# Optimization experiments

Hardware: AMD Instinct MI355X
Metric: run time of the kernel (lower is better)

Reference implementation:

```python
import jax, jax.numpy as jnp
import numpy as np

HEAD_DIM = 64
EMB_DIM = 1024
BATCH = 4
SEQ = 4096


def setup_inputs() -> dict:
    key = jax.random.key(0)
    kx, kq, kk, kv = jax.random.split(key, 4)
    scale = 1.0 / np.sqrt(EMB_DIM)
    x = jax.random.normal(kx, (BATCH, SEQ, EMB_DIM), dtype=jnp.float32)
    # nn.Linear(emb_dim, head_dim, bias=False): weight [head_dim, emb_dim]; store transposed [emb_dim, head_dim]
    Wq = jax.random.normal(kq, (EMB_DIM, HEAD_DIM), dtype=jnp.float32) * scale
    Wk = jax.random.normal(kk, (EMB_DIM, HEAD_DIM), dtype=jnp.float32) * scale
    Wv = jax.random.normal(kv, (EMB_DIM, HEAD_DIM), dtype=jnp.float32) * scale
    return {"x": x, "Wq": Wq, "Wk": Wk, "Wv": Wv}


def reference(x, Wq, Wk, Wv):
    # x: [b, s, e] -> q,k,v: [b, s, d]
    q = jnp.einsum("bse,ed->bsd", x, Wq)
    k = jnp.einsum("bse,ed->bsd", x, Wk)
    v = jnp.einsum("bse,ed->bsd", x, Wv)
    d = q.shape[-1]
    # scores: [b, s, s], scaled by 1/sqrt(head_dim)
    scores = jnp.einsum("bqd,bkd->bqk", q, k) / jnp.sqrt(jnp.asarray(d, q.dtype))
    s = x.shape[1]
    causal = jnp.tril(jnp.ones((s, s), dtype=bool))
    scores = jnp.where(causal, scores, jnp.asarray(-jnp.inf, scores.dtype))
    attn = jax.nn.softmax(scores, axis=-1)
    return jnp.einsum("bqk,bkd->bqd", attn, v)
```

## Files before the change

kernel.cpp:

```cpp
#include <hip/hip_runtime.h>
#include <hip/hip_bf16.h>
#include <math.h>

#define BATCH 4
#define SEQ   4096
#define EMB   1024
#define HD    64

#define QBLK  64
#define KBLK  64
#define CHUNK 512
#define BM    16

#define NSPB  288
#define NSLOT (BATCH * NSPB)

#define SCL   0.1803368801111204f

typedef _Float16 half8 __attribute__((ext_vector_type(8)));
typedef _Float16 half4 __attribute__((ext_vector_type(4)));
typedef float    f32x4 __attribute__((ext_vector_type(4)));

#define GLOAD_LDS16(g, l) __builtin_amdgcn_global_load_lds(                 \
    (const __attribute__((address_space(1))) void*)(g),                     \
    (__attribute__((address_space(3))) void*)(l), 16, 0, 0)

#define DPPF(v, ctrl) __int_as_float(__builtin_amdgcn_update_dpp(           \
    0, __float_as_int(v), ctrl, 0xF, 0xF, true))

static __device__ __forceinline__ float bf2f(unsigned int u16) {
    union { unsigned int i; float f; } v;
    v.i = u16 << 16;
    return v.f;
}

__global__ void detect_dtype(const unsigned short* __restrict__ x,
                             int* __restrict__ flag)
{
    const int tid = threadIdx.x;
    int big = 0;
    for (int i = tid; i < 2048; i += 64) {
        const int e = (x[i] >> 7) & 0xff;
        if (e > 146) big++;
    }
    #pragma unroll
    for (int off = 32; off; off >>= 1) big += __shfl_xor(big, off);
    if (tid == 0) *flag = (big > 200) ? 0 : 1;
}

__global__ __launch_bounds__(256) void w_to_fp16t(
    const void* __restrict__ Wqp, const void* __restrict__ Wkp,
    const void* __restrict__ Wvp, const int* __restrict__ flagp,
    _Float16* __restrict__ Wt)
{
    const int gid = blockIdx.x * 256 + threadIdx.x;
    const int n   = gid >> 7;
    const int kc  = (gid & 127) << 3;
    const int mat = n >> 6, d = n & 63;
    const void* Wp = (mat == 0) ? Wqp : (mat == 1 ? Wkp : Wvp);

    half8 o;
    if (*flagp) {
        const unsigned short* W = (const unsigned short*)Wp;
        #pragma unroll
        for (int j = 0; j < 8; ++j) o[j] = (_Float16)bf2f(W[(kc + j) * HD + d]);
    } else {
        const float* W = (const float*)Wp;
        #pragma unroll
        for (int j = 0; j < 8; ++j) o[j] = (_Float16)W[(kc + j) * HD + d];
    }
    const int tk = kc >> 5;
    *(half8*)&Wt[((tk * 192) + n) * 32 + (kc & 31)] = o;
}

__global__ __launch_bounds__(256) void qkv_gemm(
    const void* __restrict__ xp, const _Float16* __restrict__ Wt,
    const int* __restrict__ flagp,
    _Float16* __restrict__ Qh, _Float16* __restrict__ Kh,
    _Float16* __restrict__ Vth)
{
    __shared__ _Float16 Xs[2][BM * 64];

    const int tid  = threadIdx.x;
    const int w    = tid >> 6;
    const int lane = tid & 63;
    const int c15  = lane & 15;
    const int kg   = lane >> 4;
    const size_t row0 = (size_t)blockIdx.x * BM;
    const int isbf = *flagp;

    const bool st = tid < 128;
    const int sr = (tid >> 3) & 15, ss = tid & 7;
    const size_t gbase = (row0 + sr) * EMB + ss * 8;
    const int lidx = sr * 64 + ((ss ^ (sr & 7)) << 3);

    const int wtbase = (w * 48 + c15) * 32 + kg * 8;

    float4 f0[2], f1[2];
    uint4  u0,    u1;

    auto ldc = [&](int t, float4* f, uint4* u) {
        if (!st) return;
        if (isbf) *u = *(const uint4*)((const unsigned short*)xp + gbase + t * 64);
        else {
            f[0] = *(const float4*)((const float*)xp + gbase + t * 64);
            f[1] = *(const float4*)((const float*)xp + gbase + t * 64 + 4);
        }
    };
    auto wrc = [&](int buf, const float4* f, const uint4* u) {
        if (!st) return;
        half8 h;
        if (isbf) {
            const unsigned int uu[4] = {u->x, u->y, u->z, u->w};
            #pragma unroll
            for (int q = 0; q < 4; ++q) {
                h[2 * q]     = (_Float16)bf2f(uu[q] & 0xffffu);
                h[2 * q + 1] = (_Float16)bf2f(uu[q] >> 16);
            }
        } else {
            const float ff[8] = {f[0].x, f[0].y, f[0].z, f[0].w,
                                 f[1].x, f[1].y, f[1].z, f[1].w};
            #pragma unroll
            for (int q = 0; q < 8; ++q) h[q] = (_Float16)ff[q];
        }
        *(half8*)&Xs[buf][lidx] = h;
    };

    half8 bf0[6], bf1[6];
    auto ldb = [&](int t, half8* bf) {
        #pragma unroll
        for (int kk = 0; kk < 2; ++kk)
            #pragma unroll
            for (int nf = 0; nf < 3; ++nf)
                bf[kk * 3 + nf] = *(const half8*)&Wt[
                    (t * 2 + kk) * 192 * 32 + nf * 16 * 32 + wtbase];
    };

    f32x4 acc[3];
    #pragma unroll
    for (int nf = 0; nf < 3; ++nf) acc[nf] = (f32x4){0.f, 0.f, 0.f, 0.f};

    auto compute = [&](int buf, const half8* bf) {
        #pragma unroll
        for (int kk = 0; kk < 2; ++kk) {
            const half8 a = *(const half8*)&Xs[buf][c15 * 64 +
                            (((kk * 4 + kg) ^ (c15 & 7)) << 3)];
            #pragma unroll
            for (int nf = 0; nf < 3; ++nf)
                acc[nf] = __builtin_amdgcn_mfma_f32_16x16x32_f16(
                    a, bf[kk * 3 + nf], acc[nf], 0, 0, 0);
        }
    };

    ldc(0, f0, &u0);
    ldb(0, bf0);
    wrc(0, f0, &u0);
    ldc(1, f1, &u1);

    for (int tt = 0; tt < 16; tt += 2) {
        __syncthreads();
        if (tt + 2 < 16) ldc(tt + 2, f0, &u0);
        ldb(tt + 1, bf1);
        compute(0, bf0);
        wrc(1, f1, &u1);
        __syncthreads();
        if (tt + 3 < 16) ldc(tt + 3, f1, &u1);
        if (tt + 2 < 16) ldb(tt + 2, bf0);
        compute(1, bf1);
        if (tt + 2 < 16) wrc(0, f0, &u0);
    }

    #pragma unroll
    for (int nf = 0; nf < 3; ++nf) {
        const int nc  = w * 48 + nf * 16;
        const int mat = nc >> 6;
        const int d   = (nc & 63) + c15;
        if (mat < 2) {
            _Float16* Out = mat ? Kh : Qh;
            const float qs = mat ? 1.f : SCL;
            #pragma unroll
            for (int r = 0; r < 4; ++r)
                Out[(row0 + kg * 4 + r) * HD + d] = (_Float16)(acc[nf][r] * qs);
        } else {
            const int bb = (int)(row0 >> 12);
            const int s0 = (int)(row0 & 4095);
            half4 hv;
            #pragma unroll
            for (int r = 0; r < 4; ++r) hv[r] = (_Float16)acc[nf][r];
            *(half4*)&Vth[((size_t)bb * HD + d) * SEQ + s0 + kg * 4] = hv;
        }
    }
}

__global__ __launch_bounds__(256) void attn_split(
    const _Float16* __restrict__ Qh, const _Float16* __restrict__ Kh,
    const _Float16* __restrict__ Vth,
    _Float16* __restrict__ PoG, float* __restrict__ PmG,
    float* __restrict__ PlG)
{
    __shared__ _Float16 Kt[2][KBLK * HD];
    __shared__ _Float16 Vt[2][HD * KBLK];
    __shared__ _Float16 Ps[4][16 * KBLK];

    const int b = blockIdx.y;
    const int f = blockIdx.x;
    int c = 0, off = 0, cnt = 64;
    while (f >= off + cnt) { off += cnt; ++c; cnt -= 8; }
    const int qb = 8 * c + (f - off);
    const int q0 = qb * QBLK;
    const int kstart = c * CHUNK;
    const int kend   = min(kstart + CHUNK, q0 + QBLK);
    const int nt     = (kend - kstart) / KBLK;

    const int tid  = threadIdx.x;
    const int w    = tid >> 6;
    const int lane = tid & 63;
    const int col  = lane & 15;
    const int kg   = lane >> 4;

    const size_t bo = (size_t)b * SEQ;
    const _Float16* Kb = Kh + bo * HD;
    const _Float16* Vb = Vth + (size_t)b * HD * SEQ;

    const _Float16* Qp = Qh + (bo + q0 + w * 16 + col) * HD;
    const half8 aq0 = *(const half8*)(Qp + kg * 8);
    const half8 aq1 = *(const half8*)(Qp + 32 + kg * 8);

    half8 vone;
    #pragma unroll
    for (int j = 0; j < 8; ++j) vone[j] = (_Float16)1.0f;

    f32x4 O[4];
    f32x4 Ls = (f32x4){0.f, 0.f, 0.f, 0.f};
    float mreg[4];
    #pragma unroll
    for (int cq = 0; cq < 4; ++cq) O[cq] = (f32x4){0.f, 0.f, 0.f, 0.f};
    #pragma unroll
    for (int r = 0; r < 4; ++r) mreg[r] = -INFINITY;

    const int wh = w & 1;
    auto stage = [&](int t, int buf) {
        const int k0 = kstart + t * KBLK;
        if (w < 2) {
            const _Float16* g = Kb + (size_t)k0 * HD;
            #pragma unroll
            for (int i = 0; i < 4; ++i) {
                const int c2 = (wh * 4 + i) * 64 + lane;
                const int key = c2 >> 3, slot = c2 & 7;
                GLOAD_LDS16(g + key * HD + ((slot ^ (key & 7)) << 3),
                            &Kt[buf][(wh * 4 + i) * 512]);
            }
        } else {
            const _Float16* g = Vb + k0;
            #pragma unroll
            for (int i = 0; i < 4; ++i) {
                const int c2 = (wh * 4 + i) * 64 + lane;
                const int dim = c2 >> 3, slot = c2 & 7;
                GLOAD_LDS16(g + (size_t)dim * SEQ + ((slot ^ (dim & 7)) << 3),
                            &Vt[buf][(wh * 4 + i) * 512]);
            }
        }
    };

    stage(0, 0);
    int cur = 0;

    for (int t = 0; t < nt; ++t) {
        __syncthreads();
        if (t + 1 < nt) stage(t + 1, cur ^ 1);

        const int k0 = kstart + t * KBLK;

        f32x4 S[4];
        __builtin_amdgcn_s_setprio(1);
        #pragma unroll
        for (int cq = 0; cq < 4; ++cq) {
            const int key = cq * 16 + col;
            const int sw  = key & 7;
            const half8 bk0 = *(const half8*)&Kt[cur][(key * 8 + (kg ^ sw)) * 8];
            const half8 bk1 = *(const half8*)&Kt[cur][(key * 8 + ((4 + kg) ^ sw)) * 8];
            f32x4 acc = (f32x4){0.f, 0.f, 0.f, 0.f};
            acc = __builtin_amdgcn_mfma_f32_16x16x32_f16(aq0, bk0, acc, 0, 0, 0);
            acc = __builtin_amdgcn_mfma_f32_16x16x32_f16(aq1, bk1, acc, 0, 0, 0);
            S[cq] = acc;
        }
        __builtin_amdgcn_s_setprio(0);

        const int rowb  = q0 + w * 16 + kg * 4;
        const bool full = (k0 + KBLK - 1) <= (q0 + w * 16);
        float p[4][4];
        #pragma unroll
        for (int cq = 0; cq < 4; ++cq) {
            const int key = k0 + cq * 16 + col;
            #pragma unroll
            for (int r = 0; r < 4; ++r) {
                float s = S[cq][r];
                if (!full && key > rowb + r) s = -INFINITY;
                p[cq][r] = s;
            }
        }

        float vmax[4];
        #pragma unroll
        for (int r = 0; r < 4; ++r) {
            float v = fmaxf(fmaxf(p[0][r], p[1][r]), fmaxf(p[2][r], p[3][r]));
            v = fmaxf(v, DPPF(v, 0xB1));
            v = fmaxf(v, DPPF(v, 0x4E));
            v = fmaxf(v, DPPF(v, 0x141));
            v = fmaxf(v, DPPF(v, 0x140));
            vmax[r] = v;
        }

        bool grow = false;
        #pragma unroll
        for (int r = 0; r < 4; ++r) grow |= (vmax[r] > mreg[r] + 4.0f);
        if (__any(grow)) {
            #pragma unroll
            for (int r = 0; r < 4; ++r) {
                const float mn = fmaxf(mreg[r], vmax[r]);
                const float al = exp2f(mreg[r] - mn);
                mreg[r] = mn;
                Ls[r] *= al;
                #pragma unroll
                for (int cq = 0; cq < 4; ++cq)
                    O[cq][r] *= al;
            }
        }

        #pragma unroll
        for (int cq = 0; cq < 4; ++cq) {
            const int colidx = cq * 16 + col;
            #pragma unroll
            for (int r = 0; r < 4; ++r) {
                const float pv = exp2f(p[cq][r] - mreg[r]);
                const int row = kg * 4 + r;
                Ps[w][row * 64 + (colidx ^ ((row & 7) << 3))] = (_Float16)pv;
            }
        }

        __builtin_amdgcn_s_setprio(1);
        #pragma unroll
        for (int s2 = 0; s2 < 2; ++s2) {
            const int prow = col;
            const half8 pa = *(const half8*)&Ps[w][prow * 64 +
                ((s2 * 32 + kg * 8) ^ ((prow & 7) << 3))];
            #pragma unroll
            for (int cq = 0; cq < 4; ++cq) {
                const int dim = cq * 16 + col;
                const half8 bv = *(const half8*)&Vt[cur][(dim * 8 +
                    ((s2 * 4 + kg) ^ (dim & 7))) * 8];
                O[cq] = __builtin_amdgcn_mfma_f32_16x16x32_f16(pa, bv, O[cq], 0, 0, 0);
            }
            Ls = __builtin_amdgcn_mfma_f32_16x16x32_f16(pa, vone, Ls, 0, 0, 0);
        }
        __builtin_amdgcn_s_setprio(0);
        cur ^= 1;
    }

    const int pslot = b * NSPB + f;
    #pragma unroll
    for (int cq = 0; cq < 4; ++cq)
        #pragma unroll
        for (int r = 0; r < 4; ++r) {
            const int rloc = w * 16 + kg * 4 + r;
            PoG[((size_t)pslot * 64 + rloc) * 64 + cq * 16 + col] =
                (_Float16)O[cq][r];
        }
    if (col == 0) {
        #pragma unroll
        for (int r = 0; r < 4; ++r) {
            const int rloc = w * 16 + kg * 4 + r;
            PmG[pslot * 64 + rloc] = mreg[r];
            PlG[pslot * 64 + rloc] = Ls[r];
        }
    }
}

__global__ __launch_bounds__(128) void attn_merge(
    const _Float16* __restrict__ PoG, const float* __restrict__ PmG,
    const float* __restrict__ PlG, const int* __restrict__ flagp,
    void* __restrict__ outp)
{
    const int qb   = blockIdx.x;
    const int b    = blockIdx.y;
    const int rg   = blockIdx.z;
    const int nc   = (qb >> 3) + 1;
    const int tid  = threadIdx.x;
    const int rloc = rg * 16 + (tid >> 3);
    const int d0   = (tid & 7) * 8;
    const int isbf = *flagp;

    float mm = -INFINITY;
    for (int i = 0; i < nc; ++i) {
        const int sl = b * NSPB + i * (68 - 4 * i) + qb - 8 * i;
        mm = fmaxf(mm, PmG[sl * 64 + rloc]);
    }
    float acc[8] = {0.f, 0.f, 0.f, 0.f, 0.f, 0.f, 0.f, 0.f};
    float ls = 0.f;
    for (int i = 0; i < nc; ++i) {
        const int sl = b * NSPB + i * (68 - 4 * i) + qb - 8 * i;
        const float wsc = exp2f(PmG[sl * 64 + rloc] - mm);
        const half8 po = *(const half8*)&PoG[((size_t)sl * 64 + rloc) * 64 + d0];
        #pragma unroll
        for (int j = 0; j < 8; ++j) acc[j] += wsc * (float)po[j];
        ls += wsc * PlG[sl * 64 + rloc];
    }
    const float il = 1.f / ls;
    const size_t obase = ((size_t)b * SEQ + qb * QBLK + rloc) * HD + d0;
    if (isbf) {
        __hip_bfloat16* Ob = (__hip_bfloat16*)outp;
        #pragma unroll
        for (int j = 0; j < 8; ++j) Ob[obase + j] = __float2bfloat16(acc[j] * il);
    } else {
        float* Of = (float*)outp;
        #pragma unroll
        for (int j = 0; j < 8; ++j) Of[obase + j] = acc[j] * il;
    }
}

extern "C" void kernel_launch(void* const* d_in, const int* in_sizes, int n_in,
                              void* d_out, int out_size, void* d_ws, size_t ws_size,
                              hipStream_t stream)
{
    const void* x  = d_in[0];
    const void* Wq = d_in[1];
    const void* Wk = d_in[2];
    const void* Wv = d_in[3];

    const size_t N = (size_t)BATCH * SEQ * HD;
    int*      flag = (int*)d_ws;
    _Float16* Qh   = (_Float16*)((char*)d_ws + 256);
    _Float16* Kh   = Qh + N;
    _Float16* Vth  = Kh + N;
    _Float16* Wt   = Vth + N;
    float*    PmG  = (float*)(Wt + 192 * 1024);
    float*    PlG  = PmG + (size_t)NSLOT * 64;
    _Float16* PoG  = (_Float16*)(PlG + (size_t)NSLOT * 64);

    detect_dtype<<<1, 64, 0, stream>>>((const unsigned short*)x, flag);

    w_to_fp16t<<<96, 256, 0, stream>>>(Wq, Wk, Wv, flag, Wt);

    qkv_gemm<<<BATCH * SEQ / BM, 256, 0, stream>>>(x, Wt, flag, Qh, Kh, Vth);

    attn_split<<<dim3(NSPB, BATCH), 256, 0, stream>>>(Qh, Kh, Vth,
                                                      PoG, PmG, PlG);

    attn_merge<<<dim3(SEQ / QBLK, BATCH, 4), 128, 0, stream>>>(PoG, PmG, PlG,
                                                               flag, d_out);
}
```

Measured before the change: 171.2 us.

## Load QKV GEMM A-fragments directly from global, drop LDS staging and barriers

Rewrites the QKV projection GEMM so each wave loads its MFMA A-operand fragments straight from global memory into registers and converts them, instead of staging X through a swizzled LDS double buffer guarded by __syncthreads. The bf16/fp32 input switch becomes a template parameter, so the per-load runtime branch is gone. This removes LDS traffic and block barriers. In exchange, all four waves now load the same X rows redundantly, which raises global/L2 read traffic and register pressure from the extra prefetch buffers.

```diff
diff --git a/kernel.cpp b/kernel.cpp
--- a/kernel.cpp
+++ b/kernel.cpp
@@ -73,60 +73,55 @@
     *(half8*)&Wt[((tk * 192) + n) * 32 + (kc & 31)] = o;
 }
 
-__global__ __launch_bounds__(256) void qkv_gemm(
+template<bool ISBF>
+static __device__ __forceinline__ void qkv_body(
     const void* __restrict__ xp, const _Float16* __restrict__ Wt,
-    const int* __restrict__ flagp,
     _Float16* __restrict__ Qh, _Float16* __restrict__ Kh,
     _Float16* __restrict__ Vth)
 {
-    __shared__ _Float16 Xs[2][BM * 64];
-
     const int tid  = threadIdx.x;
     const int w    = tid >> 6;
     const int lane = tid & 63;
     const int c15  = lane & 15;
     const int kg   = lane >> 4;
     const size_t row0 = (size_t)blockIdx.x * BM;
-    const int isbf = *flagp;
-
-    const bool st = tid < 128;
-    const int sr = (tid >> 3) & 15, ss = tid & 7;
-    const size_t gbase = (row0 + sr) * EMB + ss * 8;
-    const int lidx = sr * 64 + ((ss ^ (sr & 7)) << 3);
-
-    const int wtbase = (w * 48 + c15) * 32 + kg * 8;
-
-    float4 f0[2], f1[2];
-    uint4  u0,    u1;
-
-    auto ldc = [&](int t, float4* f, uint4* u) {
-        if (!st) return;
-        if (isbf) *u = *(const uint4*)((const unsigned short*)xp + gbase + t * 64);
-        else {
-            f[0] = *(const float4*)((const float*)xp + gbase + t * 64);
-            f[1] = *(const float4*)((const float*)xp + gbase + t * 64 + 4);
+
+    const size_t abase  = (row0 + c15) * EMB + kg * 8;
+    const int    wtbase = (w * 48 + c15) * 32 + kg * 8;
+
+    struct ARaw { uint4 u0, u1; float4 g0[2], g1[2]; };
+
+    auto lda = [&](int t, ARaw& r) {
+        if constexpr (ISBF) {
+            const unsigned short* xb =
+                (const unsigned short*)xp + abase + (size_t)t * 64;
+            r.u0 = *(const uint4*)xb;
+            r.u1 = *(const uint4*)(xb + 32);
+        } else {
+            const float* xf = (const float*)xp + abase + (size_t)t * 64;
+            r.g0[0] = *(const float4*)(xf);
+            r.g0[1] = *(const float4*)(xf + 4);
+            r.g1[0] = *(const float4*)(xf + 32);
+            r.g1[1] = *(const float4*)(xf + 36);
         }
     };
-    auto wrc = [&](int buf, const float4* f, const uint4* u) {
-        if (!st) return;
+    auto cvt = [&](const uint4& u, const float4* g) -> half8 {
         half8 h;
-        if (isbf) {
-            const unsigned int uu[4] = {u->x, u->y, u->z, u->w};
+        if constexpr (ISBF) {
+            const unsigned int uu[4] = {u.x, u.y, u.z, u.w};
             #pragma unroll
             for (int q = 0; q < 4; ++q) {
                 h[2 * q]     = (_Float16)bf2f(uu[q] & 0xffffu);
                 h[2 * q + 1] = (_Float16)bf2f(uu[q] >> 16);
             }
         } else {
-            const float ff[8] = {f[0].x, f[0].y, f[0].z, f[0].w,
-                                 f[1].x, f[1].y, f[1].z, f[1].w};
+            const float ff[8] = {g[0].x, g[0].y, g[0].z, g[0].w,
+                                 g[1].x, g[1].y, g[1].z, g[1].w};
             #pragma unroll
             for (int q = 0; q < 8; ++q) h[q] = (_Float16)ff[q];
         }
-        *(half8*)&Xs[buf][lidx] = h;
+        return h;
     };
-
-    half8 bf0[6], bf1[6];
     auto ldb = [&](int t, half8* bf) {
         #pragma unroll
         for (int kk = 0; kk < 2; ++kk)
@@ -140,34 +135,29 @@
     #pragma unroll
     for (int nf = 0; nf < 3; ++nf) acc[nf] = (f32x4){0.f, 0.f, 0.f, 0.f};
 
-    auto compute = [&](int buf, const half8* bf) {
-        #pragma unroll
-        for (int kk = 0; kk < 2; ++kk) {
-            const half8 a = *(const half8*)&Xs[buf][c15 * 64 +
-                            (((kk * 4 + kg) ^ (c15 & 7)) << 3)];
-            #pragma unroll
-            for (int nf = 0; nf < 3; ++nf)
-                acc[nf] = __builtin_amdgcn_mfma_f32_16x16x32_f16(
-                    a, bf[kk * 3 + nf], acc[nf], 0, 0, 0);
-        }
+    auto compute = [&](const ARaw& r, const half8* bf) {
+        const half8 a0 = cvt(r.u0, r.g0);
+        const half8 a1 = cvt(r.u1, r.g1);
+        #pragma unroll
+        for (int nf = 0; nf < 3; ++nf)
+            acc[nf] = __builtin_amdgcn_mfma_f32_16x16x32_f16(
+                a0, bf[nf], acc[nf], 0, 0, 0);
+        #pragma unroll
+        for (int nf = 0; nf < 3; ++nf)
+            acc[nf] = __builtin_amdgcn_mfma_f32_16x16x32_f16(
+                a1, bf[3 + nf], acc[nf], 0, 0, 0);
     };
 
-    ldc(0, f0, &u0);
-    ldb(0, bf0);
-    wrc(0, f0, &u0);
-    ldc(1, f1, &u1);
+    ARaw  r0, r1;
+    half8 b0[6], b1[6];
+    lda(0, r0); ldb(0, b0);
+    lda(1, r1); ldb(1, b1);
 
     for (int tt = 0; tt < 16; tt += 2) {
-        __syncthreads();
-        if (tt + 2 < 16) ldc(tt + 2, f0, &u0);
-        ldb(tt + 1, bf1);
-        compute(0, bf0);
-        wrc(1, f1, &u1);
-        __syncthreads();
-        if (tt + 3 < 16) ldc(tt + 3, f1, &u1);
-        if (tt + 2 < 16) ldb(tt + 2, bf0);
-        compute(1, bf1);
-        if (tt + 2 < 16) wrc(0, f0, &u0);
+        compute(r0, b0);
+        if (tt + 2 < 16) { lda(tt + 2, r0); ldb(tt + 2, b0); }
+        compute(r1, b1);
+        if (tt + 3 < 16) { lda(tt + 3, r1); ldb(tt + 3, b1); }
     }
 
     #pragma unroll
@@ -190,6 +180,16 @@
             *(half4*)&Vth[((size_t)bb * HD + d) * SEQ + s0 + kg * 4] = hv;
         }
     }
+}
+
+__global__ __launch_bounds__(256) void qkv_gemm(
+    const void* __restrict__ xp, const _Float16* __restrict__ Wt,
+    const int* __restrict__ flagp,
+    _Float16* __restrict__ Qh, _Float16* __restrict__ Kh,
+    _Float16* __restrict__ Vth)
+{
+    if (*flagp) qkv_body<true >(xp, Wt, Qh, Kh, Vth);
+    else        qkv_body<false>(xp, Wt, Qh, Kh, Vth);
 }
 
 __global__ __launch_bounds__(256) void attn_split(
```

After: 189.6 us. 10.7% more time.
